# Performance work log

Measured on AMD Instinct MI355X. Metric: run time of the kernel, lower is better.

Reference implementation:

```python
import jax, jax.numpy as jnp
import numpy as np

DIM = 128
NUM_HEADS = 4
WINDOW = (2, 7, 7)  # Wh, Ww, Wd -> n = 98
N_TOK = WINDOW[0] * WINDOW[1] * WINDOW[2]
RPB_ROWS = (2 * WINDOW[0] - 1) * (2 * WINDOW[1] - 1) * (2 * WINDOW[2] - 1)  # 507
B_ = 2048   # num_windows * batch
NW = 64     # windows per image (mask leading dim); B_ % NW == 0


def setup_inputs() -> dict:
    key = jax.random.key(0)
    k_x, k_rpi, k_tab, k_w = jax.random.split(key, 4)
    x = jax.random.normal(k_x, (B_, N_TOK, 3 * DIM), dtype=jnp.float32)
    rpi = jax.random.randint(k_rpi, (N_TOK, N_TOK), 0, RPB_ROWS, dtype=jnp.int64)
    mask = jnp.zeros((NW, N_TOK, N_TOK), dtype=jnp.float32)
    rpb_table = 0.02 * jax.random.normal(k_tab, (RPB_ROWS, NUM_HEADS), dtype=jnp.float32)
    proj_w = jax.random.normal(k_w, (DIM, DIM), dtype=jnp.float32) * (DIM ** -0.5)
    proj_b = jnp.zeros((DIM,), dtype=jnp.float32)
    return {"x": x, "rpi": rpi, "mask": mask, "rpb_table": rpb_table,
            "proj_w": proj_w, "proj_b": proj_b}


def reference(x, rpi, mask, rpb_table, proj_w, proj_b):
    b_, n, c = x.shape
    h = NUM_HEADS
    hd = c // h // 3                     # head_dim = dim // num_heads
    scale = hd ** -0.5
    qkv = x.reshape(b_, n, 3, h, hd).transpose(2, 0, 3, 1, 4)
    q, k, v = qkv[0], qkv[1], qkv[2]
    attn = jnp.einsum('bhqd,bhkd->bhqk', q * scale, k)  # (b_, h, n, n)
    # gathered relative position bias: (n, n, h) -> (h, n, n)
    bias = rpb_table[rpi.reshape(-1)].reshape(n, n, h).transpose(2, 0, 1)
    attn = attn + bias[None]
    # additive window mask: (nw, n, n) broadcast over batch-of-images and heads
    nw = mask.shape[0]
    attn = attn.reshape(b_ // nw, nw, h, n, n) + mask[None, :, None]
    attn = jax.nn.softmax(attn.reshape(b_, h, n, n), axis=-1)
    out = jnp.einsum('bhqk,bhkd->bhqd', attn, v)         # (b_, h, n, hd)
    out = out.transpose(0, 2, 1, 3).reshape(b_, n, h * hd)
    return out @ proj_w.T + proj_b
```

## Files before the change

### kernel.cpp

```cpp
#include <hip/hip_runtime.h>

typedef __attribute__((ext_vector_type(8))) short short8;
typedef __attribute__((ext_vector_type(4))) float f32x4;

#define N_TOK 98
#define HD    32
#define NH    4
#define DIM   128
#define C3    384
#define NWIN  64
#define B_TOT 2048
#define MT    112
#define SCALE 0.17677669529663687f
#define CSHIFT 8.0f

#define SQK    40
#define SPS    136
#define SVS    136
#define K_OFF  8960
#define VT_OFF 30464
#define LDSZ   39168

#define BIAS_ELEMS (NH * MT * MT)
#define WPERM_ELEMS (NH * 8 * 4 * 16 * 8)
#define WPERM_BYTE_OFF 200704
#define OBF_BYTE_OFF   233472
#define OBF_BYTES ((size_t)B_TOT * N_TOK * DIM * 2)

__device__ __forceinline__ short f2bf(float f) {
    unsigned u = __builtin_bit_cast(unsigned, f);
    u += 0x7fffu + ((u >> 16) & 1u);
    return (short)(u >> 16);
}

__global__ void prep_kernel(const int* __restrict__ rpi,
                            const float* __restrict__ rpb,
                            const float* __restrict__ wmat,
                            float* __restrict__ biasD,
                            short* __restrict__ wperm) {
    int idx = blockIdx.x * 256 + threadIdx.x;
    if (idx < BIAS_ELEMS) {
        int j = idx % MT, rest = idx / MT;
        int i = rest % MT, h = rest / MT;
        float v = 0.f;
        if (i < N_TOK && j < N_TOK) v = rpb[rpi[i * N_TOK + j] * NH + h];
        biasD[idx] = v;
    } else if (idx < BIAS_ELEMS + WPERM_ELEMS) {
        int e = idx - BIAS_ELEMS;
        int k = e & 7, r2 = e >> 3;
        int c = r2 & 15; r2 >>= 4;
        int q = r2 & 3;  r2 >>= 2;
        int nt = r2 & 7; int h = r2 >> 3;
        wperm[e] = f2bf(wmat[(nt * 16 + c) * DIM + h * HD + q * 8 + k]);
    }
}

__global__ __launch_bounds__(448, 7) void attn_kernel(
    const float* __restrict__ x, const float* __restrict__ mask,
    const float* __restrict__ biasD, float* __restrict__ out,
    short* __restrict__ obf, const int use_bf)
{
    __shared__ __align__(16) char smem[LDSZ];
    short* sQ  = (short*)smem;
    short* sK  = (short*)(smem + K_OFF);
    short* sP  = (short*)smem;
    short* sVT = (short*)(smem + VT_OFF);

    const int t  = threadIdx.x;
    const int bh = blockIdx.x;
    const int b  = bh >> 2, h = bh & 3;
    const int w  = b & (NWIN - 1);
    const float* xb = x + (size_t)b * N_TOK * C3;

    const int lane = t & 63;
    const int c    = lane & 15, q = lane >> 4;
    const int m0   = (t >> 6) * 16;

    for (int e = t; e < MT * 8; e += 448) {
        int row = e >> 3, d4 = (e & 7) << 2;
        unsigned long long qp = 0ull, kp = 0ull;
        if (row < N_TOK) {
            const float* p = xb + row * C3 + h * HD + d4;
            float4 qv = *(const float4*)p;
            float4 kv = *(const float4*)(p + DIM);
            qp =  (unsigned long long)(unsigned short)f2bf(qv.x * SCALE)
               | ((unsigned long long)(unsigned short)f2bf(qv.y * SCALE) << 16)
               | ((unsigned long long)(unsigned short)f2bf(qv.z * SCALE) << 32)
               | ((unsigned long long)(unsigned short)f2bf(qv.w * SCALE) << 48);
            kp =  (unsigned long long)(unsigned short)f2bf(kv.x)
               | ((unsigned long long)(unsigned short)f2bf(kv.y) << 16)
               | ((unsigned long long)(unsigned short)f2bf(kv.z) << 32)
               | ((unsigned long long)(unsigned short)f2bf(kv.w) << 48);
        }
        *(unsigned long long*)&sQ[row * SQK + d4] = qp;
        *(unsigned long long*)&sK[row * SQK + d4] = kp;
    }
    for (int e = t; e < N_TOK * 8; e += 448) {
        int j = e >> 3, d4 = (e & 7) << 2;
        float4 vv = *(const float4*)(xb + j * C3 + 2 * DIM + h * HD + d4);
        sVT[(d4 + 0) * SVS + j] = f2bf(vv.x);
        sVT[(d4 + 1) * SVS + j] = f2bf(vv.y);
        sVT[(d4 + 2) * SVS + j] = f2bf(vv.z);
        sVT[(d4 + 3) * SVS + j] = f2bf(vv.w);
    }
    for (int e = t; e < HD * (SVS - N_TOK); e += 448) {
        int d = e / (SVS - N_TOK), j = N_TOK + e % (SVS - N_TOK);
        sVT[d * SVS + j] = 0;
    }

    f32x4 cfrag[7];
    #pragma unroll
    for (int nt = 0; nt < 7; ++nt) {
        int j = nt * 16 + c;
        #pragma unroll
        for (int r = 0; r < 4; ++r) {
            int i = m0 + q * 4 + r;
            float cf;
            if (j < N_TOK) {
                cf = biasD[(h * MT + i) * MT + j] - CSHIFT;
                if (i < N_TOK)
                    cf += mask[((size_t)w * N_TOK + i) * N_TOK + j];
            } else cf = -1e30f;
            cfrag[nt][r] = cf;
        }
    }
    __syncthreads();

    short8 afrag = *(const short8*)&sQ[(m0 + c) * SQK + q * 8];
    f32x4 acc[7];
    #pragma unroll
    for (int nt = 0; nt < 7; ++nt) {
        short8 bfrag = *(const short8*)&sK[(nt * 16 + c) * SQK + q * 8];
        acc[nt] = __builtin_amdgcn_mfma_f32_16x16x32_bf16(afrag, bfrag, cfrag[nt], 0, 0, 0);
    }
    __syncthreads();

    float sm[4] = {0.f, 0.f, 0.f, 0.f};
    #pragma unroll
    for (int nt = 0; nt < 7; ++nt) {
        int j = nt * 16 + c;
        #pragma unroll
        for (int r = 0; r < 4; ++r) {
            int i = m0 + q * 4 + r;
            float e = __expf(acc[nt][r]);
            sm[r] += e;
            sP[i * SPS + j] = f2bf(e);
        }
    }
    #pragma unroll
    for (int kk = 0; kk < 4; ++kk)
        sP[(m0 + c) * SPS + 112 + q * 4 + kk] = 0;
    float inv[4];
    #pragma unroll
    for (int r = 0; r < 4; ++r) {
        float s = sm[r];
        s += __shfl_xor(s, 1);
        s += __shfl_xor(s, 2);
        s += __shfl_xor(s, 4);
        s += __shfl_xor(s, 8);
        inv[r] = 1.0f / s;
    }

    f32x4 oacc[2] = {{0.f,0.f,0.f,0.f}, {0.f,0.f,0.f,0.f}};
    #pragma unroll
    for (int kt = 0; kt < 4; ++kt) {
        short8 pa = *(const short8*)&sP[(m0 + c) * SPS + kt * 32 + q * 8];
        #pragma unroll
        for (int n2 = 0; n2 < 2; ++n2) {
            short8 vb = *(const short8*)&sVT[(n2 * 16 + c) * SVS + kt * 32 + q * 8];
            oacc[n2] = __builtin_amdgcn_mfma_f32_16x16x32_bf16(pa, vb, oacc[n2], 0, 0, 0);
        }
    }

    if (use_bf) {
        #pragma unroll
        for (int n2 = 0; n2 < 2; ++n2)
            #pragma unroll
            for (int r = 0; r < 4; ++r) {
                int i = m0 + q * 4 + r;
                if (i < N_TOK)
                    obf[((size_t)b * N_TOK + i) * DIM + h * HD + n2 * 16 + c]
                        = f2bf(oacc[n2][r] * inv[r]);
            }
    } else {
        #pragma unroll
        for (int n2 = 0; n2 < 2; ++n2)
            #pragma unroll
            for (int r = 0; r < 4; ++r) {
                int i = m0 + q * 4 + r;
                if (i < N_TOK)
                    out[((size_t)b * N_TOK + i) * DIM + h * HD + n2 * 16 + c]
                        = oacc[n2][r] * inv[r];
            }
    }
}

#define PR 112
__global__ __launch_bounds__(448) void proj_bf(
    const short* __restrict__ obf, const short* __restrict__ wperm,
    const float* __restrict__ pbias, float* __restrict__ out)
{
    const int t = threadIdx.x;
    const int lane = t & 63;
    const int c = lane & 15, q = lane >> 4;
    const int m0 = (t >> 6) * 16;
    const size_t r0 = (size_t)blockIdx.x * PR;

    f32x4 acc[8];
    #pragma unroll
    for (int nt = 0; nt < 8; ++nt) acc[nt] = (f32x4){0.f, 0.f, 0.f, 0.f};

    #pragma unroll
    for (int kt = 0; kt < 4; ++kt) {
        short8 a = *(const short8*)&obf[(r0 + m0 + c) * DIM + kt * 32 + q * 8];
        #pragma unroll
        for (int nt = 0; nt < 8; ++nt) {
            short8 wb = *(const short8*)&wperm[(((kt * 8 + nt) * 4 + q) * 16 + c) * 8];
            acc[nt] = __builtin_amdgcn_mfma_f32_16x16x32_bf16(a, wb, acc[nt], 0, 0, 0);
        }
    }
    #pragma unroll
    for (int nt = 0; nt < 8; ++nt) {
        float bc = pbias[nt * 16 + c];
        #pragma unroll
        for (int r = 0; r < 4; ++r)
            out[(r0 + m0 + q * 4 + r) * DIM + nt * 16 + c] = acc[nt][r] + bc;
    }
}

__global__ __launch_bounds__(448) void proj_f32(
    const float* __restrict__ wmat, const float* __restrict__ bias,
    float* __restrict__ io)
{
    __shared__ short sX[PR][136];
    __shared__ short sW[DIM][136];
    const int t = threadIdx.x;
    const size_t r0 = (size_t)blockIdx.x * PR;

    for (int e = t; e < PR * 32; e += 448) {
        int rr = e >> 5, k4 = (e & 31) << 2;
        float4 v = *(const float4*)&io[(r0 + rr) * DIM + k4];
        sX[rr][k4 + 0] = f2bf(v.x);
        sX[rr][k4 + 1] = f2bf(v.y);
        sX[rr][k4 + 2] = f2bf(v.z);
        sX[rr][k4 + 3] = f2bf(v.w);
    }
    for (int e = t; e < DIM * 32; e += 448) {
        int rr = e >> 5, k4 = (e & 31) << 2;
        float4 v = *(const float4*)&wmat[rr * DIM + k4];
        sW[rr][k4 + 0] = f2bf(v.x);
        sW[rr][k4 + 1] = f2bf(v.y);
        sW[rr][k4 + 2] = f2bf(v.z);
        sW[rr][k4 + 3] = f2bf(v.w);
    }
    __syncthreads();

    const int lane = t & 63;
    const int c = lane & 15, q = lane >> 4;
    const int mt = t >> 6;

    float bcol[8];
    #pragma unroll
    for (int nt = 0; nt < 8; ++nt) bcol[nt] = bias[nt * 16 + c];

    f32x4 acc[8];
    #pragma unroll
    for (int nt = 0; nt < 8; ++nt) acc[nt] = (f32x4){0.f, 0.f, 0.f, 0.f};

    #pragma unroll
    for (int kt = 0; kt < 4; ++kt) {
        short8 a = *(const short8*)&sX[mt * 16 + c][kt * 32 + q * 8];
        #pragma unroll
        for (int nt = 0; nt < 8; ++nt) {
            short8 bb = *(const short8*)&sW[nt * 16 + c][kt * 32 + q * 8];
            acc[nt] = __builtin_amdgcn_mfma_f32_16x16x32_bf16(a, bb, acc[nt], 0, 0, 0);
        }
    }
    #pragma unroll
    for (int nt = 0; nt < 8; ++nt)
        #pragma unroll
        for (int r = 0; r < 4; ++r)
            io[(r0 + mt * 16 + q * 4 + r) * DIM + nt * 16 + c] = acc[nt][r] + bcol[nt];
}

extern "C" void kernel_launch(void* const* d_in, const int* in_sizes, int n_in,
                              void* d_out, int out_size, void* d_ws, size_t ws_size,
                              hipStream_t stream) {
    const float* x    = (const float*)d_in[0];
    const int*   rpi  = (const int*)  d_in[1];
    const float* mask = (const float*)d_in[2];
    const float* rpb  = (const float*)d_in[3];
    const float* pw   = (const float*)d_in[4];
    const float* pb   = (const float*)d_in[5];
    float* out   = (float*)d_out;
    float* biasD = (float*)d_ws;
    short* wperm = (short*)((char*)d_ws + WPERM_BYTE_OFF);
    short* obf   = (short*)((char*)d_ws + OBF_BYTE_OFF);

    const int use_bf = (ws_size >= OBF_BYTE_OFF + OBF_BYTES) ? 1 : 0;

    prep_kernel<<<(BIAS_ELEMS + WPERM_ELEMS + 255) / 256, 256, 0, stream>>>(
        rpi, rpb, pw, biasD, wperm);
    attn_kernel<<<B_TOT * NH, 448, 0, stream>>>(x, mask, biasD, out, obf, use_bf);
    if (use_bf)
        proj_bf<<<(B_TOT * N_TOK) / PR, 448, 0, stream>>>(obf, wperm, pb, out);
    else
        proj_f32<<<(B_TOT * N_TOK) / PR, 448, 0, stream>>>(pw, pb, out);
}
```

Before: 607.5 us.

## Loop heads per window block with prefetch and precombined bias-mask table

```diff
diff --git a/kernel.cpp b/kernel.cpp
--- a/kernel.cpp
+++ b/kernel.cpp
@@ -21,11 +21,15 @@
 #define VT_OFF 30464
 #define LDSZ   39168
 
-#define BIAS_ELEMS (NH * MT * MT)
 #define WPERM_ELEMS (NH * 8 * 4 * 16 * 8)
-#define WPERM_BYTE_OFF 200704
-#define OBF_BYTE_OFF   233472
-#define OBF_BYTES ((size_t)B_TOT * N_TOK * DIM * 2)
+#define BIAS_OFF    32768
+#define BIAS_ELEMS  (NH * MT * MT)
+#define CMB_OFF     233472
+#define CMB_ELEMS   (NWIN * NH * 7 * 7 * 64 * 4)
+#define OBF_FULL_OFF 13078528
+#define OBF_BYTES   ((size_t)B_TOT * N_TOK * DIM * 2)
+#define FULL_BYTES  (OBF_FULL_OFF + OBF_BYTES)
+#define OBF_FB_OFF  233472
 
 __device__ __forceinline__ short f2bf(float f) {
     unsigned u = __builtin_bit_cast(unsigned, f);
@@ -36,26 +40,216 @@
 __global__ void prep_kernel(const int* __restrict__ rpi,
                             const float* __restrict__ rpb,
                             const float* __restrict__ wmat,
+                            const float* __restrict__ mask,
+                            short* __restrict__ wperm,
                             float* __restrict__ biasD,
-                            short* __restrict__ wperm) {
+                            float* __restrict__ cmb, const int do_cmb) {
     int idx = blockIdx.x * 256 + threadIdx.x;
-    if (idx < BIAS_ELEMS) {
-        int j = idx % MT, rest = idx / MT;
-        int i = rest % MT, h = rest / MT;
-        float v = 0.f;
-        if (i < N_TOK && j < N_TOK) v = rpb[rpi[i * N_TOK + j] * NH + h];
-        biasD[idx] = v;
-    } else if (idx < BIAS_ELEMS + WPERM_ELEMS) {
-        int e = idx - BIAS_ELEMS;
+    if (idx < WPERM_ELEMS) {
+        int e = idx;
         int k = e & 7, r2 = e >> 3;
         int c = r2 & 15; r2 >>= 4;
         int q = r2 & 3;  r2 >>= 2;
         int nt = r2 & 7; int h = r2 >> 3;
         wperm[e] = f2bf(wmat[(nt * 16 + c) * DIM + h * HD + q * 8 + k]);
-    }
-}
-
-__global__ __launch_bounds__(448, 7) void attn_kernel(
+    } else if (idx < WPERM_ELEMS + BIAS_ELEMS) {
+        int e = idx - WPERM_ELEMS;
+        int j = e % MT, rest = e / MT;
+        int i = rest % MT, h = rest / MT;
+        float v = 0.f;
+        if (i < N_TOK && j < N_TOK) v = rpb[rpi[i * N_TOK + j] * NH + h];
+        biasD[e] = v;
+    } else if (do_cmb) {
+        int e = idx - (WPERM_ELEMS + BIAS_ELEMS);
+        if (e < CMB_ELEMS) {
+            int r = e & 3, ln = (e >> 2) & 63;
+            int g = e >> 8;
+            int nt = g % 7; g /= 7;
+            int mt = g % 7; g /= 7;
+            int h = g & 3, ww = g >> 2;
+            int i = mt * 16 + (ln >> 4) * 4 + r;
+            int j = nt * 16 + (ln & 15);
+            float v = -1e30f;
+            if (i < N_TOK && j < N_TOK)
+                v = rpb[rpi[i * N_TOK + j] * NH + h]
+                  + mask[((size_t)ww * N_TOK + i) * N_TOK + j] - CSHIFT;
+            cmb[e] = v;
+        }
+    }
+}
+
+__global__ __launch_bounds__(448, 6) void attn_pipe(
+    const float* __restrict__ x, const float* __restrict__ cmb,
+    short* __restrict__ obf)
+{
+    __shared__ __align__(16) char smem[LDSZ];
+    short* sQ  = (short*)smem;
+    short* sK  = (short*)(smem + K_OFF);
+    short* sP  = (short*)smem;
+    short* sVT = (short*)(smem + VT_OFF);
+
+    const int t = threadIdx.x;
+    const int b = blockIdx.x;
+    const int w = b & (NWIN - 1);
+    const float* xb = x + (size_t)b * N_TOK * C3;
+
+    const int lane  = t & 63;
+    const int c     = lane & 15, q = lane >> 4;
+    const int mtile = t >> 6;
+    const int m0    = mtile * 16;
+
+    const int row0 = t >> 3, d40 = (t & 7) << 2;
+    const int row1 = row0 + 56;
+    const bool r1ok = row1 < N_TOK;
+    const int vj0 = row0, vd0 = d40;
+    const int vj1 = vj0 + 56;
+    const bool v1ok = vj1 < N_TOK;
+
+    float4 qv0 = {0,0,0,0}, kv0 = {0,0,0,0};
+    float4 qv1 = {0,0,0,0}, kv1 = {0,0,0,0};
+    float4 vv0 = {0,0,0,0}, vv1 = {0,0,0,0};
+
+    {
+        const float* base = xb;
+        const float* p0 = base + row0 * C3 + d40;
+        qv0 = *(const float4*)p0;
+        kv0 = *(const float4*)(p0 + DIM);
+        if (r1ok) {
+            const float* p1 = base + row1 * C3 + d40;
+            qv1 = *(const float4*)p1;
+            kv1 = *(const float4*)(p1 + DIM);
+        }
+        vv0 = *(const float4*)(base + vj0 * C3 + 2 * DIM + vd0);
+        if (v1ok) vv1 = *(const float4*)(base + vj1 * C3 + 2 * DIM + vd0);
+    }
+    for (int e = t; e < HD * (SVS - N_TOK); e += 448) {
+        int d = e / (SVS - N_TOK), j = N_TOK + e % (SVS - N_TOK);
+        sVT[d * SVS + j] = 0;
+    }
+
+    #pragma unroll 1
+    for (int h = 0; h < NH; ++h) {
+        __syncthreads();
+
+        {
+            unsigned long long qp0 =
+                  (unsigned long long)(unsigned short)f2bf(qv0.x * SCALE)
+               | ((unsigned long long)(unsigned short)f2bf(qv0.y * SCALE) << 16)
+               | ((unsigned long long)(unsigned short)f2bf(qv0.z * SCALE) << 32)
+               | ((unsigned long long)(unsigned short)f2bf(qv0.w * SCALE) << 48);
+            unsigned long long kp0 =
+                  (unsigned long long)(unsigned short)f2bf(kv0.x)
+               | ((unsigned long long)(unsigned short)f2bf(kv0.y) << 16)
+               | ((unsigned long long)(unsigned short)f2bf(kv0.z) << 32)
+               | ((unsigned long long)(unsigned short)f2bf(kv0.w) << 48);
+            *(unsigned long long*)&sQ[row0 * SQK + d40] = qp0;
+            *(unsigned long long*)&sK[row0 * SQK + d40] = kp0;
+            unsigned long long qp1 = 0ull, kp1 = 0ull;
+            if (r1ok) {
+                qp1 =  (unsigned long long)(unsigned short)f2bf(qv1.x * SCALE)
+                   | ((unsigned long long)(unsigned short)f2bf(qv1.y * SCALE) << 16)
+                   | ((unsigned long long)(unsigned short)f2bf(qv1.z * SCALE) << 32)
+                   | ((unsigned long long)(unsigned short)f2bf(qv1.w * SCALE) << 48);
+                kp1 =  (unsigned long long)(unsigned short)f2bf(kv1.x)
+                   | ((unsigned long long)(unsigned short)f2bf(kv1.y) << 16)
+                   | ((unsigned long long)(unsigned short)f2bf(kv1.z) << 32)
+                   | ((unsigned long long)(unsigned short)f2bf(kv1.w) << 48);
+            }
+            *(unsigned long long*)&sQ[row1 * SQK + d40] = qp1;
+            *(unsigned long long*)&sK[row1 * SQK + d40] = kp1;
+            sVT[(vd0 + 0) * SVS + vj0] = f2bf(vv0.x);
+            sVT[(vd0 + 1) * SVS + vj0] = f2bf(vv0.y);
+            sVT[(vd0 + 2) * SVS + vj0] = f2bf(vv0.z);
+            sVT[(vd0 + 3) * SVS + vj0] = f2bf(vv0.w);
+            if (v1ok) {
+                sVT[(vd0 + 0) * SVS + vj1] = f2bf(vv1.x);
+                sVT[(vd0 + 1) * SVS + vj1] = f2bf(vv1.y);
+                sVT[(vd0 + 2) * SVS + vj1] = f2bf(vv1.z);
+                sVT[(vd0 + 3) * SVS + vj1] = f2bf(vv1.w);
+            }
+        }
+
+        const float* cb = cmb
+            + ((size_t)((w * NH + h) * 7 + mtile) * 7) * 256 + lane * 4;
+        f32x4 cf[7];
+        #pragma unroll
+        for (int nt = 0; nt < 7; ++nt)
+            cf[nt] = *(const f32x4*)(cb + nt * 256);
+
+        __syncthreads();
+
+        short8 afrag = *(const short8*)&sQ[(m0 + c) * SQK + q * 8];
+        f32x4 acc[7];
+        #pragma unroll
+        for (int nt = 0; nt < 7; ++nt) {
+            short8 bfrag = *(const short8*)&sK[(nt * 16 + c) * SQK + q * 8];
+            acc[nt] = __builtin_amdgcn_mfma_f32_16x16x32_bf16(afrag, bfrag, cf[nt], 0, 0, 0);
+        }
+        __syncthreads();
+
+        if (h + 1 < NH) {
+            const float* base = xb + (h + 1) * HD;
+            const float* p0 = base + row0 * C3 + d40;
+            qv0 = *(const float4*)p0;
+            kv0 = *(const float4*)(p0 + DIM);
+            if (r1ok) {
+                const float* p1 = base + row1 * C3 + d40;
+                qv1 = *(const float4*)p1;
+                kv1 = *(const float4*)(p1 + DIM);
+            }
+            vv0 = *(const float4*)(base + vj0 * C3 + 2 * DIM + vd0);
+            if (v1ok) vv1 = *(const float4*)(base + vj1 * C3 + 2 * DIM + vd0);
+        }
+
+        float sm[4] = {0.f, 0.f, 0.f, 0.f};
+        #pragma unroll
+        for (int nt = 0; nt < 7; ++nt) {
+            int j = nt * 16 + c;
+            #pragma unroll
+            for (int r = 0; r < 4; ++r) {
+                int i = m0 + q * 4 + r;
+                float e = __expf(acc[nt][r]);
+                sm[r] += e;
+                sP[i * SPS + j] = f2bf(e);
+            }
+        }
+        #pragma unroll
+        for (int kk = 0; kk < 4; ++kk)
+            sP[(m0 + c) * SPS + 112 + q * 4 + kk] = 0;
+        float inv[4];
+        #pragma unroll
+        for (int r = 0; r < 4; ++r) {
+            float s = sm[r];
+            s += __shfl_xor(s, 1);
+            s += __shfl_xor(s, 2);
+            s += __shfl_xor(s, 4);
+            s += __shfl_xor(s, 8);
+            inv[r] = 1.0f / s;
+        }
+
+        f32x4 oacc[2] = {{0.f,0.f,0.f,0.f}, {0.f,0.f,0.f,0.f}};
+        #pragma unroll
+        for (int kt = 0; kt < 4; ++kt) {
+            short8 pa = *(const short8*)&sP[(m0 + c) * SPS + kt * 32 + q * 8];
+            #pragma unroll
+            for (int n2 = 0; n2 < 2; ++n2) {
+                short8 vb = *(const short8*)&sVT[(n2 * 16 + c) * SVS + kt * 32 + q * 8];
+                oacc[n2] = __builtin_amdgcn_mfma_f32_16x16x32_bf16(pa, vb, oacc[n2], 0, 0, 0);
+            }
+        }
+        #pragma unroll
+        for (int n2 = 0; n2 < 2; ++n2)
+            #pragma unroll
+            for (int r = 0; r < 4; ++r) {
+                int i = m0 + q * 4 + r;
+                if (i < N_TOK)
+                    obf[((size_t)b * N_TOK + i) * DIM + h * HD + n2 * 16 + c]
+                        = f2bf(oacc[n2][r] * inv[r]);
+            }
+    }
+}
+
+__global__ __launch_bounds__(448, 7) void attn_fb(
     const float* __restrict__ x, const float* __restrict__ mask,
     const float* __restrict__ biasD, float* __restrict__ out,
     short* __restrict__ obf, const int use_bf)
@@ -171,7 +365,6 @@
             oacc[n2] = __builtin_amdgcn_mfma_f32_16x16x32_bf16(pa, vb, oacc[n2], 0, 0, 0);
         }
     }
-
     if (use_bf) {
         #pragma unroll
         for (int n2 = 0; n2 < 2; ++n2)
@@ -293,17 +486,26 @@
     const float* pw   = (const float*)d_in[4];
     const float* pb   = (const float*)d_in[5];
     float* out   = (float*)d_out;
-    float* biasD = (float*)d_ws;
-    short* wperm = (short*)((char*)d_ws + WPERM_BYTE_OFF);
-    short* obf   = (short*)((char*)d_ws + OBF_BYTE_OFF);
-
-    const int use_bf = (ws_size >= OBF_BYTE_OFF + OBF_BYTES) ? 1 : 0;
-
-    prep_kernel<<<(BIAS_ELEMS + WPERM_ELEMS + 255) / 256, 256, 0, stream>>>(
-        rpi, rpb, pw, biasD, wperm);
-    attn_kernel<<<B_TOT * NH, 448, 0, stream>>>(x, mask, biasD, out, obf, use_bf);
-    if (use_bf)
+    short* wperm = (short*)d_ws;
+    float* biasD = (float*)((char*)d_ws + BIAS_OFF);
+    float* cmb   = (float*)((char*)d_ws + CMB_OFF);
+
+    const int full = (ws_size >= FULL_BYTES) ? 1 : 0;
+    short* obf = (short*)((char*)d_ws + (full ? OBF_FULL_OFF : OBF_FB_OFF));
+    const int fb_bf = (ws_size >= OBF_FB_OFF + OBF_BYTES) ? 1 : 0;
+
+    const int prep_elems = WPERM_ELEMS + BIAS_ELEMS + (full ? CMB_ELEMS : 0);
+    prep_kernel<<<(prep_elems + 255) / 256, 256, 0, stream>>>(
+        rpi, rpb, pw, mask, wperm, biasD, cmb, full);
+
+    if (full) {
+        attn_pipe<<<B_TOT, 448, 0, stream>>>(x, cmb, obf);
         proj_bf<<<(B_TOT * N_TOK) / PR, 448, 0, stream>>>(obf, wperm, pb, out);
-    else
-        proj_f32<<<(B_TOT * N_TOK) / PR, 448, 0, stream>>>(pw, pb, out);
-}
+    } else {
+        attn_fb<<<B_TOT * NH, 448, 0, stream>>>(x, mask, biasD, out, obf, fb_bf);
+        if (fb_bf)
+            proj_bf<<<(B_TOT * N_TOK) / PR, 448, 0, stream>>>(obf, wperm, pb, out);
+        else
+            proj_f32<<<(B_TOT * N_TOK) / PR, 448, 0, stream>>>(pw, pb, out);
+    }
+}
```

Result: faster. 542.1 us (-10.8%).
